# Performance work log

Hardware: AMD Instinct MI355X
Metric: run time of the kernel (lower is better)

Reference implementation:

```python
import jax, jax.numpy as jnp
import numpy as np

B, S, D, H = 4, 2048, 1024, 16
HD = D // H  # 64


def setup_inputs() -> dict:
    key = jax.random.key(0)
    ks = jax.random.split(key, 9)
    s = 1.0 / np.sqrt(D)
    return {
        "x": jax.random.normal(ks[0], (B, S, D), dtype=jnp.float32),
        "Wq": jax.random.normal(ks[1], (D, D), dtype=jnp.float32) * s,
        "bq": jax.random.normal(ks[2], (D,), dtype=jnp.float32) * 0.01,
        "Wk": jax.random.normal(ks[3], (D, D), dtype=jnp.float32) * s,
        "bk": jax.random.normal(ks[4], (D,), dtype=jnp.float32) * 0.01,
        "Wv": jax.random.normal(ks[5], (D, D), dtype=jnp.float32) * s,
        "bv": jax.random.normal(ks[6], (D,), dtype=jnp.float32) * 0.01,
        "Wo": jax.random.normal(ks[7], (D, D), dtype=jnp.float32) * s,
        "bo": jax.random.normal(ks[8], (D,), dtype=jnp.float32) * 0.01,
    }


def reference(x, Wq, bq, Wk, bk, Wv, bv, Wo, bo):
    b, s, _ = x.shape
    # projections -> [b, h, s, hd]
    def proj(W, bias):
        return (x @ W.T + bias).reshape(b, s, H, HD).transpose(0, 2, 1, 3)
    q, k, v = proj(Wq, bq), proj(Wk, bk), proj(Wv, bv)
    # NOTE: source multiplies by sqrt(head_dim)**0.5 = head_dim**0.25 (quirk kept)
    scale = jnp.asarray(HD, dtype=x.dtype) ** 0.25
    scores = jnp.einsum("bhqd,bhkd->bhqk", q, k) * scale
    causal = jnp.tril(jnp.ones((s, s), dtype=bool))
    scores = jnp.where(causal, scores, -jnp.inf)
    attn = jax.nn.softmax(scores, axis=-1)  # dropout p=0 (eval) -> identity
    out = jnp.einsum("bhqk,bhkd->bhqd", attn, v)
    out = out.transpose(0, 2, 1, 3).reshape(b, s, D)
    return out @ Wo.T + bo
```

## Files before the change

### kernel.cpp

```cpp
#include <hip/hip_runtime.h>
#include <hip/hip_fp16.h>


typedef unsigned short u16;
typedef _Float16 half8 __attribute__((ext_vector_type(8)));
typedef float f32x4 __attribute__((ext_vector_type(4)));
typedef unsigned short ushort8 __attribute__((ext_vector_type(8)));
typedef unsigned short us4 __attribute__((ext_vector_type(4)));

#define LOG2E 1.4426950408889634f
#define SCL2 4.0816663172343815f
#define SWZ(r) ((((r) ^ ((r) >> 3))) & 7)

__device__ __forceinline__ u16 f2h(float f) {
  return __half_as_ushort(__float2half(f));
}

__device__ __forceinline__ void gload16(const void* gsrc, void* ldst) {
  typedef __attribute__((address_space(1))) const void glob_t;
  typedef __attribute__((address_space(3))) void lds_t;
  __builtin_amdgcn_global_load_lds((glob_t*)gsrc, (lds_t*)ldst, 16, 0, 0);
}

__device__ __forceinline__ f32x4 mfma_f16(half8 a, half8 b, f32x4 c) {
  return __builtin_amdgcn_mfma_f32_16x16x32_f16(a, b, c, 0, 0, 0);
}

__global__ __launch_bounds__(256) void cvt_f32_f16(const float* __restrict__ in,
                                                   u16* __restrict__ out, int n8) {
  int i = blockIdx.x * 256 + threadIdx.x;
  if (i >= n8) return;
  const float4* p = (const float4*)in + (size_t)i * 2;
  float4 a = p[0], b = p[1];
  ushort8 v;
  v[0] = f2h(a.x); v[1] = f2h(a.y); v[2] = f2h(a.z); v[3] = f2h(a.w);
  v[4] = f2h(b.x); v[5] = f2h(b.y); v[6] = f2h(b.z); v[7] = f2h(b.w);
  *(ushort8*)(out + (size_t)i * 8) = v;
}

__device__ __forceinline__ void gemm_body(const u16* __restrict__ A, const u16* __restrict__ Bw,
                                          const float* __restrict__ bias,
                                          u16* __restrict__ Ch, float* __restrict__ Cf,
                                          u16* __restrict__ Vtp) {
  __shared__ __align__(16) u16 sA[128 * 32];
  __shared__ __align__(16) u16 sB[128 * 32];
  const int m0 = blockIdx.y * 128, n0 = blockIdx.x * 128;
  const int tid = threadIdx.x, w = tid >> 6, l = tid & 63;
  const int wm = (w >> 1) * 64, wn = (w & 1) * 64;
  f32x4 acc[4][4] = {};
  const int srow = tid >> 2, sch = (tid & 3) * 8;
  char* sAb = (char*)sA + w * 1024;
  char* sBb = (char*)sB + w * 1024;
  const u16* Ag0 = A + (size_t)(m0 + srow) * 1024 + sch;
  const u16* Ag1 = A + (size_t)(m0 + 64 + srow) * 1024 + sch;
  const u16* Bg0 = Bw + (size_t)(n0 + srow) * 1024 + sch;
  const u16* Bg1 = Bw + (size_t)(n0 + 64 + srow) * 1024 + sch;
  for (int kt = 0; kt < 32; ++kt) {
    const int k0 = kt * 32;
    __syncthreads();
    gload16(Ag0 + k0, sAb);
    gload16(Ag1 + k0, sAb + 4096);
    gload16(Bg0 + k0, sBb);
    gload16(Bg1 + k0, sBb + 4096);
    __syncthreads();
    half8 a[4], b[4];
#pragma unroll
    for (int mf = 0; mf < 4; ++mf)
      a[mf] = *(const half8*)&sA[(wm + mf * 16 + (l & 15)) * 32 + (l >> 4) * 8];
#pragma unroll
    for (int nf = 0; nf < 4; ++nf)
      b[nf] = *(const half8*)&sB[(wn + nf * 16 + (l & 15)) * 32 + (l >> 4) * 8];
#pragma unroll
    for (int mf = 0; mf < 4; ++mf)
#pragma unroll
      for (int nf = 0; nf < 4; ++nf)
        acc[mf][nf] = mfma_f16(a[mf], b[nf], acc[mf][nf]);
  }
  if (Vtp) {
#pragma unroll
    for (int nf = 0; nf < 4; ++nf) {
      const int col = n0 + wn + nf * 16 + (l & 15);
      const float bv = bias[col];
#pragma unroll
      for (int mf = 0; mf < 4; ++mf) {
        const int row = m0 + wm + mf * 16 + (l >> 4) * 4;
        us4 v;
#pragma unroll
        for (int r = 0; r < 4; ++r) v[r] = f2h(acc[mf][nf][r] + bv);
        *(us4*)(Vtp + (size_t)((row >> 11) * 16 + (col >> 6)) * 131072 +
                (size_t)(col & 63) * 2048 + (row & 2047)) = v;
      }
    }
  } else {
#pragma unroll
    for (int nf = 0; nf < 4; ++nf) {
      const int col = n0 + wn + nf * 16 + (l & 15);
      const float bv = bias[col];
#pragma unroll
      for (int mf = 0; mf < 4; ++mf) {
#pragma unroll
        for (int r = 0; r < 4; ++r) {
          const int row = m0 + wm + mf * 16 + (l >> 4) * 4 + r;
          float v = acc[mf][nf][r] + bv;
          if (Cf) Cf[(size_t)row * 1024 + col] = v;
          else    Ch[(size_t)row * 1024 + col] = f2h(v);
        }
      }
    }
  }
}

struct QkvArgs {
  const u16* B[3];
  const float* bias[3];
  u16* C[3];
};

__global__ __launch_bounds__(256) void gemm_qkv(const u16* __restrict__ A, QkvArgs ga) {
  const int z = blockIdx.z;
  if (z == 2) gemm_body(A, ga.B[2], ga.bias[2], nullptr, nullptr, ga.C[2]);
  else        gemm_body(A, ga.B[z], ga.bias[z], ga.C[z], nullptr, nullptr);
}

__global__ __launch_bounds__(256) void gemm_out(const u16* __restrict__ A, const u16* __restrict__ Bw,
                                                const float* __restrict__ bias, float* __restrict__ C) {
  gemm_body(A, Bw, bias, nullptr, C, nullptr);
}

__global__ __launch_bounds__(256) void attn_fused(const u16* __restrict__ Qb, const u16* __restrict__ Kb,
                                                  const u16* __restrict__ Vt, u16* __restrict__ Ob) {
  __shared__ __align__(16) u16 k_s[64 * 64];
  __shared__ __align__(16) u16 vt_s[64 * 64];
  __shared__ __align__(16) u16 p_s[4 * 16 * 64];
  const int bid = blockIdx.x;
  const int bh = bid & 63;
  const int qt = 31 - (bid >> 6);
  const int b = bh >> 4, h = bh & 15;
  const size_t baseQ = (size_t)b * 2048 * 1024 + h * 64;
  const size_t baseV = (size_t)(b * 16 + h) * 131072;
  const int q0 = qt * 64;
  const int tid = threadIdx.x, w = tid >> 6, l = tid & 63;
  const int g = l >> 4, qi = l & 15;
  const int q_loc = w * 16 + qi;
  const int q_glob = q0 + q_loc;

  half8 qf0, qf1;
  {
    const u16* qp = Qb + baseQ + (size_t)q_glob * 1024 + g * 8;
    qf0 = *(const half8*)(qp);
    qf1 = *(const half8*)(qp + 32);
  }
  const int srow = w * 8 + (l >> 3);
  const int sch0 = (l & 7) ^ SWZ(srow);
  const int sch1 = (l & 7) ^ SWZ(srow + 32);
  const u16* pK0 = Kb + baseQ + (size_t)srow * 1024 + sch0 * 8;
  const u16* pK1 = Kb + baseQ + (size_t)(srow + 32) * 1024 + sch1 * 8;
  const u16* pV0 = Vt + baseV + (size_t)srow * 2048 + sch0 * 8;
  const u16* pV1 = Vt + baseV + (size_t)(srow + 32) * 2048 + sch1 * 8;
  char* kd0 = (char*)k_s + w * 1024;
  char* kd1 = (char*)k_s + 4096 + w * 1024;
  char* vd0 = (char*)vt_s + w * 1024;
  char* vd1 = (char*)vt_s + 4096 + w * 1024;
  int koff[4], pvoff[2];
#pragma unroll
  for (int nf = 0; nf < 4; ++nf) {
    const int row = nf * 16 + qi;
    koff[nf] = row * 64 + ((g ^ SWZ(row)) << 3);
  }
#pragma unroll
  for (int ks = 0; ks < 2; ++ks)
    pvoff[ks] = qi * 64 + (((ks * 4 + g) ^ SWZ(qi)) << 3);
  u16* pw = p_s + w * 1024;

  f32x4 s[4], o[4] = {};
  float m_r = -INFINITY, l_r = 0.f;

  for (int kt = 0; kt <= qt; ++kt) {
    __syncthreads();
    gload16(pK0, kd0);
    gload16(pK1, kd1);
    gload16(pV0, vd0);
    gload16(pV1, vd1);
    pK0 += 65536; pK1 += 65536; pV0 += 64; pV1 += 64;
    __syncthreads();
#pragma unroll
    for (int nf = 0; nf < 4; ++nf) {
      half8 k0 = *(const half8*)(k_s + koff[nf]);
      half8 k1 = *(const half8*)(k_s + (koff[nf] ^ 32));
      f32x4 acc = {};
      acc = mfma_f16(k0, qf0, acc);
      acc = mfma_f16(k1, qf1, acc);
      s[nf] = acc * SCL2;
    }
    if (kt == qt) {
#pragma unroll
      for (int nf = 0; nf < 4; ++nf) {
        const int kb = nf * 16 + g * 4;
#pragma unroll
        for (int r = 0; r < 4; ++r)
          if (kb + r > q_loc) s[nf][r] = -INFINITY;
      }
    }
    float t = fmaxf(fmaxf(fmaxf(s[0][0], s[0][1]), fmaxf(s[0][2], s[0][3])),
                    fmaxf(fmaxf(s[1][0], s[1][1]), fmaxf(s[1][2], s[1][3])));
    t = fmaxf(t, fmaxf(fmaxf(fmaxf(s[2][0], s[2][1]), fmaxf(s[2][2], s[2][3])),
                       fmaxf(fmaxf(s[3][0], s[3][1]), fmaxf(s[3][2], s[3][3]))));
    t = fmaxf(t, __shfl_xor(t, 16));
    t = fmaxf(t, __shfl_xor(t, 32));
    const float mn = fmaxf(m_r, t);
    const float al = __builtin_amdgcn_exp2f(m_r - mn);
    float rs = 0.f;
#pragma unroll
    for (int nf = 0; nf < 4; ++nf) {
#pragma unroll
      for (int r = 0; r < 4; ++r) {
        const float p = __builtin_amdgcn_exp2f(s[nf][r] - mn);
        s[nf][r] = p;
        rs += p;
      }
    }
    rs += __shfl_xor(rs, 16);
    rs += __shfl_xor(rs, 32);
    l_r = l_r * al + rs;
    m_r = mn;
#pragma unroll
    for (int nf = 0; nf < 4; ++nf) o[nf] *= al;
#pragma unroll
    for (int nf = 0; nf < 4; ++nf) {
      us4 v;
      v[0] = f2h(s[nf][0]); v[1] = f2h(s[nf][1]);
      v[2] = f2h(s[nf][2]); v[3] = f2h(s[nf][3]);
      const int c = nf * 2 + (g >> 1);
      *(us4*)(pw + qi * 64 + ((c ^ SWZ(qi)) << 3) + (g & 1) * 4) = v;
    }
#pragma unroll
    for (int ks = 0; ks < 2; ++ks) {
      half8 pf = *(const half8*)(pw + pvoff[ks]);
#pragma unroll
      for (int nf = 0; nf < 4; ++nf) {
        const int vrow = nf * 16 + qi;
        half8 vf = *(const half8*)(vt_s + vrow * 64 + (((ks * 4 + g) ^ SWZ(vrow)) << 3));
        o[nf] = mfma_f16(vf, pf, o[nf]);
      }
    }
  }
  const float inv = 1.f / l_r;
  u16* op = Ob + (size_t)(b * 2048 + q_glob) * 1024 + h * 64 + g * 4;
#pragma unroll
  for (int nf = 0; nf < 4; ++nf) {
    us4 v;
#pragma unroll
    for (int r = 0; r < 4; ++r) v[r] = f2h(o[nf][r] * inv);
    *(us4*)(op + nf * 16) = v;
  }
}

extern "C" void kernel_launch(void* const* d_in, const int* in_sizes, int n_in,
                              void* d_out, int out_size, void* d_ws, size_t ws_size,
                              hipStream_t stream) {
  (void)in_sizes; (void)n_in; (void)out_size; (void)ws_size;
  const float* x  = (const float*)d_in[0];
  const float* Wq = (const float*)d_in[1];
  const float* bq = (const float*)d_in[2];
  const float* Wk = (const float*)d_in[3];
  const float* bk = (const float*)d_in[4];
  const float* Wv = (const float*)d_in[5];
  const float* bv = (const float*)d_in[6];
  const float* Wo = (const float*)d_in[7];
  const float* bo = (const float*)d_in[8];

  u16* xb = (u16*)d_ws;
  u16* wq = xb + (size_t)8192 * 1024;
  u16* wk = wq + 1024 * 1024;
  u16* wv = wk + 1024 * 1024;
  u16* wo = wv + 1024 * 1024;
  u16* Qb = wo + 1024 * 1024;
  u16* Kb = Qb + (size_t)8192 * 1024;
  u16* Vt = Kb + (size_t)8192 * 1024;
  u16* Ab = xb;

  cvt_f32_f16<<<4096, 256, 0, stream>>>(x, xb, 1048576);
  cvt_f32_f16<<<512, 256, 0, stream>>>(Wq, wq, 131072);
  cvt_f32_f16<<<512, 256, 0, stream>>>(Wk, wk, 131072);
  cvt_f32_f16<<<512, 256, 0, stream>>>(Wv, wv, 131072);
  cvt_f32_f16<<<512, 256, 0, stream>>>(Wo, wo, 131072);

  QkvArgs ga;
  ga.B[0] = wq; ga.B[1] = wk; ga.B[2] = wv;
  ga.bias[0] = bq; ga.bias[1] = bk; ga.bias[2] = bv;
  ga.C[0] = Qb; ga.C[1] = Kb; ga.C[2] = Vt;
  gemm_qkv<<<dim3(8, 64, 3), 256, 0, stream>>>(xb, ga);

  attn_fused<<<2048, 256, 0, stream>>>(Qb, Kb, Vt, Ab);

  gemm_out<<<dim3(8, 64), 256, 0, stream>>>(Ab, wo, bo, (float*)d_out);
}
```

Baseline: 302.7 us.

## Pair causal query tiles per block and add lazy softmax rescaling

```diff
diff --git a/kernel.cpp b/kernel.cpp
--- a/kernel.cpp
+++ b/kernel.cpp
@@ -3,17 +3,25 @@
 
 
 typedef unsigned short u16;
+typedef unsigned int u32;
 typedef _Float16 half8 __attribute__((ext_vector_type(8)));
 typedef float f32x4 __attribute__((ext_vector_type(4)));
 typedef unsigned short ushort8 __attribute__((ext_vector_type(8)));
 typedef unsigned short us4 __attribute__((ext_vector_type(4)));
-
-#define LOG2E 1.4426950408889634f
+typedef unsigned int u32x2 __attribute__((ext_vector_type(2)));
+
 #define SCL2 4.0816663172343815f
 #define SWZ(r) ((((r) ^ ((r) >> 3))) & 7)
 
 __device__ __forceinline__ u16 f2h(float f) {
   return __half_as_ushort(__float2half(f));
+}
+
+__device__ __forceinline__ us4 pack4(float a, float b, float c, float d) {
+  u32x2 t;
+  t[0] = __builtin_bit_cast(u32, __builtin_amdgcn_cvt_pkrtz(a, b));
+  t[1] = __builtin_bit_cast(u32, __builtin_amdgcn_cvt_pkrtz(c, d));
+  return __builtin_bit_cast(us4, t);
 }
 
 __device__ __forceinline__ void gload16(const void* gsrc, void* ldst) {
@@ -134,29 +142,17 @@
   __shared__ __align__(16) u16 p_s[4 * 16 * 64];
   const int bid = blockIdx.x;
   const int bh = bid & 63;
-  const int qt = 31 - (bid >> 6);
+  const int pj = bid >> 6;
   const int b = bh >> 4, h = bh & 15;
   const size_t baseQ = (size_t)b * 2048 * 1024 + h * 64;
   const size_t baseV = (size_t)(b * 16 + h) * 131072;
-  const int q0 = qt * 64;
   const int tid = threadIdx.x, w = tid >> 6, l = tid & 63;
   const int g = l >> 4, qi = l & 15;
   const int q_loc = w * 16 + qi;
-  const int q_glob = q0 + q_loc;
-
-  half8 qf0, qf1;
-  {
-    const u16* qp = Qb + baseQ + (size_t)q_glob * 1024 + g * 8;
-    qf0 = *(const half8*)(qp);
-    qf1 = *(const half8*)(qp + 32);
-  }
+
   const int srow = w * 8 + (l >> 3);
   const int sch0 = (l & 7) ^ SWZ(srow);
   const int sch1 = (l & 7) ^ SWZ(srow + 32);
-  const u16* pK0 = Kb + baseQ + (size_t)srow * 1024 + sch0 * 8;
-  const u16* pK1 = Kb + baseQ + (size_t)(srow + 32) * 1024 + sch1 * 8;
-  const u16* pV0 = Vt + baseV + (size_t)srow * 2048 + sch0 * 8;
-  const u16* pV1 = Vt + baseV + (size_t)(srow + 32) * 2048 + sch1 * 8;
   char* kd0 = (char*)k_s + w * 1024;
   char* kd1 = (char*)k_s + 4096 + w * 1024;
   char* vd0 = (char*)vt_s + w * 1024;
@@ -172,86 +168,103 @@
     pvoff[ks] = qi * 64 + (((ks * 4 + g) ^ SWZ(qi)) << 3);
   u16* pw = p_s + w * 1024;
 
-  f32x4 s[4], o[4] = {};
-  float m_r = -INFINITY, l_r = 0.f;
-
-  for (int kt = 0; kt <= qt; ++kt) {
-    __syncthreads();
-    gload16(pK0, kd0);
-    gload16(pK1, kd1);
-    gload16(pV0, vd0);
-    gload16(pV1, vd1);
-    pK0 += 65536; pK1 += 65536; pV0 += 64; pV1 += 64;
-    __syncthreads();
-#pragma unroll
-    for (int nf = 0; nf < 4; ++nf) {
-      half8 k0 = *(const half8*)(k_s + koff[nf]);
-      half8 k1 = *(const half8*)(k_s + (koff[nf] ^ 32));
-      f32x4 acc = {};
-      acc = mfma_f16(k0, qf0, acc);
-      acc = mfma_f16(k1, qf1, acc);
-      s[nf] = acc * SCL2;
+  for (int half = 0; half < 2; ++half) {
+    const int qt = half ? (31 - pj) : pj;
+    const int q0 = qt * 64;
+    const int q_glob = q0 + q_loc;
+
+    half8 qf0, qf1;
+    {
+      const u16* qp = Qb + baseQ + (size_t)q_glob * 1024 + g * 8;
+      qf0 = *(const half8*)(qp);
+      qf1 = *(const half8*)(qp + 32);
     }
-    if (kt == qt) {
+    const u16* pK0 = Kb + baseQ + (size_t)srow * 1024 + sch0 * 8;
+    const u16* pK1 = Kb + baseQ + (size_t)(srow + 32) * 1024 + sch1 * 8;
+    const u16* pV0 = Vt + baseV + (size_t)srow * 2048 + sch0 * 8;
+    const u16* pV1 = Vt + baseV + (size_t)(srow + 32) * 2048 + sch1 * 8;
+
+    f32x4 s[4], o[4] = {};
+    float m_r = -INFINITY, l_r = 0.f;
+
+    for (int kt = 0; kt <= qt; ++kt) {
+      __syncthreads();
+      gload16(pK0, kd0);
+      gload16(pK1, kd1);
+      gload16(pV0, vd0);
+      gload16(pV1, vd1);
+      pK0 += 65536; pK1 += 65536; pV0 += 64; pV1 += 64;
+      __syncthreads();
 #pragma unroll
       for (int nf = 0; nf < 4; ++nf) {
-        const int kb = nf * 16 + g * 4;
-#pragma unroll
-        for (int r = 0; r < 4; ++r)
-          if (kb + r > q_loc) s[nf][r] = -INFINITY;
+        half8 k0 = *(const half8*)(k_s + koff[nf]);
+        half8 k1 = *(const half8*)(k_s + (koff[nf] ^ 32));
+        f32x4 acc = {};
+        acc = mfma_f16(k0, qf0, acc);
+        acc = mfma_f16(k1, qf1, acc);
+        s[nf] = acc * SCL2;
+      }
+      if (kt == qt) {
+#pragma unroll
+        for (int nf = 0; nf < 4; ++nf) {
+          const int kb = nf * 16 + g * 4;
+#pragma unroll
+          for (int r = 0; r < 4; ++r)
+            if (kb + r > q_loc) s[nf][r] = -INFINITY;
+        }
+      }
+      float t = fmaxf(fmaxf(fmaxf(s[0][0], s[0][1]), s[0][2]),
+                      fmaxf(fmaxf(s[0][3], s[1][0]), s[1][1]));
+      t = fmaxf(t, fmaxf(fmaxf(s[1][2], s[1][3]), s[2][0]));
+      t = fmaxf(t, fmaxf(fmaxf(s[2][1], s[2][2]), s[2][3]));
+      t = fmaxf(t, fmaxf(fmaxf(s[3][0], s[3][1]), s[3][2]));
+      t = fmaxf(t, s[3][3]);
+      t = fmaxf(t, __shfl_xor(t, 16));
+      t = fmaxf(t, __shfl_xor(t, 32));
+      if (!__all(t <= m_r + 8.f)) {
+        const float mn = fmaxf(m_r, t);
+        const float al = __builtin_amdgcn_exp2f(m_r - mn);
+        l_r *= al;
+#pragma unroll
+        for (int nf = 0; nf < 4; ++nf) o[nf] *= al;
+        m_r = mn;
+      }
+      float rs = 0.f;
+#pragma unroll
+      for (int nf = 0; nf < 4; ++nf) {
+#pragma unroll
+        for (int r = 0; r < 4; ++r) {
+          const float p = __builtin_amdgcn_exp2f(s[nf][r] - m_r);
+          s[nf][r] = p;
+          rs += p;
+        }
+      }
+      rs += __shfl_xor(rs, 16);
+      rs += __shfl_xor(rs, 32);
+      l_r += rs;
+#pragma unroll
+      for (int nf = 0; nf < 4; ++nf) {
+        const int c = nf * 2 + (g >> 1);
+        *(us4*)(pw + qi * 64 + ((c ^ SWZ(qi)) << 3) + (g & 1) * 4) =
+            pack4(s[nf][0], s[nf][1], s[nf][2], s[nf][3]);
+      }
+#pragma unroll
+      for (int ks = 0; ks < 2; ++ks) {
+        half8 pf = *(const half8*)(pw + pvoff[ks]);
+#pragma unroll
+        for (int nf = 0; nf < 4; ++nf) {
+          const int vrow = nf * 16 + qi;
+          half8 vf = *(const half8*)(vt_s + vrow * 64 + (((ks * 4 + g) ^ SWZ(vrow)) << 3));
+          o[nf] = mfma_f16(vf, pf, o[nf]);
+        }
       }
     }
-    float t = fmaxf(fmaxf(fmaxf(s[0][0], s[0][1]), fmaxf(s[0][2], s[0][3])),
-                    fmaxf(fmaxf(s[1][0], s[1][1]), fmaxf(s[1][2], s[1][3])));
-    t = fmaxf(t, fmaxf(fmaxf(fmaxf(s[2][0], s[2][1]), fmaxf(s[2][2], s[2][3])),
-                       fmaxf(fmaxf(s[3][0], s[3][1]), fmaxf(s[3][2], s[3][3]))));
-    t = fmaxf(t, __shfl_xor(t, 16));
-    t = fmaxf(t, __shfl_xor(t, 32));
-    const float mn = fmaxf(m_r, t);
-    const float al = __builtin_amdgcn_exp2f(m_r - mn);
-    float rs = 0.f;
-#pragma unroll
-    for (int nf = 0; nf < 4; ++nf) {
-#pragma unroll
-      for (int r = 0; r < 4; ++r) {
-        const float p = __builtin_amdgcn_exp2f(s[nf][r] - mn);
-        s[nf][r] = p;
-        rs += p;
-      }
-    }
-    rs += __shfl_xor(rs, 16);
-    rs += __shfl_xor(rs, 32);
-    l_r = l_r * al + rs;
-    m_r = mn;
-#pragma unroll
-    for (int nf = 0; nf < 4; ++nf) o[nf] *= al;
-#pragma unroll
-    for (int nf = 0; nf < 4; ++nf) {
-      us4 v;
-      v[0] = f2h(s[nf][0]); v[1] = f2h(s[nf][1]);
-      v[2] = f2h(s[nf][2]); v[3] = f2h(s[nf][3]);
-      const int c = nf * 2 + (g >> 1);
-      *(us4*)(pw + qi * 64 + ((c ^ SWZ(qi)) << 3) + (g & 1) * 4) = v;
-    }
-#pragma unroll
-    for (int ks = 0; ks < 2; ++ks) {
-      half8 pf = *(const half8*)(pw + pvoff[ks]);
-#pragma unroll
-      for (int nf = 0; nf < 4; ++nf) {
-        const int vrow = nf * 16 + qi;
-        half8 vf = *(const half8*)(vt_s + vrow * 64 + (((ks * 4 + g) ^ SWZ(vrow)) << 3));
-        o[nf] = mfma_f16(vf, pf, o[nf]);
-      }
-    }
-  }
-  const float inv = 1.f / l_r;
-  u16* op = Ob + (size_t)(b * 2048 + q_glob) * 1024 + h * 64 + g * 4;
-#pragma unroll
-  for (int nf = 0; nf < 4; ++nf) {
-    us4 v;
-#pragma unroll
-    for (int r = 0; r < 4; ++r) v[r] = f2h(o[nf][r] * inv);
-    *(us4*)(op + nf * 16) = v;
+    const float inv = 1.f / l_r;
+    u16* op = Ob + (size_t)(b * 2048 + q_glob) * 1024 + h * 64 + g * 4;
+#pragma unroll
+    for (int nf = 0; nf < 4; ++nf)
+      *(us4*)(op + nf * 16) =
+          pack4(o[nf][0] * inv, o[nf][1] * inv, o[nf][2] * inv, o[nf][3] * inv);
   }
 }
 
@@ -291,7 +304,7 @@
   ga.C[0] = Qb; ga.C[1] = Kb; ga.C[2] = Vt;
   gemm_qkv<<<dim3(8, 64, 3), 256, 0, stream>>>(xb, ga);
 
-  attn_fused<<<2048, 256, 0, stream>>>(Qb, Kb, Vt, Ab);
+  attn_fused<<<1024, 256, 0, stream>>>(Qb, Kb, Vt, Ab);
 
   gemm_out<<<dim3(8, 64), 256, 0, stream>>>(Ab, wo, bo, (float*)d_out);
 }
```

New measurement: 307.9 us. Within noise of the previous version (+1.7%).
